# Kernel optimization log

Hardware: AMD Instinct MI355X
Metric: run time of the kernel (lower is better)

## Reference

```python
import jax, jax.numpy as jnp
import numpy as np

N_NODES = 100000
N_EDGES = 1600000
IN_C, HID_C, OUT_C = 32, 64, 32


def setup_inputs() -> dict:
    key = jax.random.key(0)
    ks = jax.random.split(key, 8)
    x = jax.random.normal(ks[0], (N_NODES, IN_C), dtype=jnp.float32)
    edge_index = jax.random.randint(ks[1], (2, N_EDGES), 0, N_NODES, dtype=jnp.int64)
    s = 1.0 / np.sqrt(IN_C)
    W1_l = jax.random.uniform(ks[2], (IN_C, HID_C), jnp.float32, -s, s)
    W1_r = jax.random.uniform(ks[3], (IN_C, HID_C), jnp.float32, -s, s)
    b1 = jnp.zeros((HID_C,), jnp.float32)
    s2 = 1.0 / np.sqrt(HID_C)
    W2_l = jax.random.uniform(ks[4], (HID_C, OUT_C), jnp.float32, -s2, s2)
    W2_r = jax.random.uniform(ks[5], (HID_C, OUT_C), jnp.float32, -s2, s2)
    b2 = jnp.zeros((OUT_C,), jnp.float32)
    return {"x": x, "edge_index": edge_index, "W1_l": W1_l, "b1": b1,
            "W1_r": W1_r, "W2_l": W2_l, "b2": b2, "W2_r": W2_r}


def _sage_conv(x, src, dst, W_l, b_l, W_r):
    # mean-aggregate source features onto destination nodes (PyG SAGEConv)
    n = x.shape[0]
    agg = jax.ops.segment_sum(x[src], dst, num_segments=n)  # [N, C]
    cnt = jax.ops.segment_sum(jnp.ones_like(dst, dtype=x.dtype), dst, num_segments=n)
    agg = agg / jnp.maximum(cnt, 1.0)[:, None]
    return agg @ W_l + b_l + x @ W_r


def reference(x, edge_index, W1_l, b1, W1_r, W2_l, b2, W2_r):
    src, dst = edge_index[0], edge_index[1]
    h = jax.nn.relu(_sage_conv(x, src, dst, W1_l, b1, W1_r))
    # dropout omitted (eval mode, deterministic baseline)
    out = _sage_conv(h, src, dst, W2_l, b2, W2_r)
    return out
```

## Files before the change

kernel.cpp:

```cpp
#include <hip/hip_runtime.h>
#include <hip/hip_bf16.h>


#define BUCKET_SHIFT 8
#define BUCKET_SPAN  256
#define BUCKET_CAP   8192
#define PART_ITEMS   32
#define PART_TILE    (256 * PART_ITEMS)

__global__ __launch_bounds__(256) void partition_kernel(
        const int* __restrict__ src, const int* __restrict__ dst,
        int* __restrict__ cursorB, int* __restrict__ edgesB, int E, int nbuck) {
    __shared__ int hist[512];
    __shared__ int rank_[512];
    __shared__ int base[512];
    const int tid = threadIdx.x;
    const int tbase = blockIdx.x * PART_TILE;

    for (int i = tid; i < 512; i += 256) { hist[i] = 0; rank_[i] = 0; }
    __syncthreads();

#pragma unroll
    for (int it = 0; it < PART_ITEMS; ++it) {
        int idx = tbase + it * 256 + tid;
        if (idx < E) atomicAdd(&hist[dst[idx] >> BUCKET_SHIFT], 1);
    }
    __syncthreads();

    for (int i = tid; i < nbuck; i += 256) {
        int h = hist[i];
        base[i] = h ? atomicAdd(&cursorB[i], h) : 0;
    }
    __syncthreads();

#pragma unroll
    for (int it = 0; it < PART_ITEMS; ++it) {
        int idx = tbase + it * 256 + tid;
        if (idx < E) {
            int d = dst[idx];
            int b = d >> BUCKET_SHIFT;
            int ld = d & (BUCKET_SPAN - 1);
            int r = atomicAdd(&rank_[b], 1);
            edgesB[(size_t)b * BUCKET_CAP + base[b] + r] = (ld << 24) | src[idx];
        }
    }
}

__global__ __launch_bounds__(512) void bucket_scan_kernel(
        const int* __restrict__ cursorB, int* __restrict__ bucketStart, int nbuck) {
    __shared__ int s[512];
    int t = threadIdx.x;
    int v = (t < nbuck) ? cursorB[t] : 0;
    s[t] = v;
    __syncthreads();
    for (int off = 1; off < 512; off <<= 1) {
        int a = (t >= off) ? s[t - off] : 0;
        __syncthreads();
        s[t] += a;
        __syncthreads();
    }
    if (t < nbuck) bucketStart[t] = s[t] - v;
}

__global__ __launch_bounds__(256) void bucket_csr_kernel(
        const int* __restrict__ cursorB, const int* __restrict__ bucketStart,
        const int* __restrict__ edgesB, int* __restrict__ row_start,
        int* __restrict__ sorted_src, int N, int nbuck) {
    __shared__ int cnt[BUCKET_SPAN];
    __shared__ int cur[BUCKET_SPAN];
    __shared__ int sc[BUCKET_SPAN];
    __shared__ int sorted[BUCKET_CAP];

    const int b = blockIdx.x;
    const int t = threadIdx.x;
    const int nodeBase = b << BUCKET_SHIFT;
    const int span = min(BUCKET_SPAN, N - nodeBase);
    const int size = cursorB[b];
    const int gstart = bucketStart[b];
    const int* eb = edgesB + (size_t)b * BUCKET_CAP;

    cnt[t] = 0;
    __syncthreads();
    for (int i = t; i < size; i += 256) atomicAdd(&cnt[((unsigned)eb[i]) >> 24], 1);
    __syncthreads();

    sc[t] = cnt[t];
    __syncthreads();
    for (int off = 1; off < BUCKET_SPAN; off <<= 1) {
        int a = (t >= off) ? sc[t - off] : 0;
        __syncthreads();
        sc[t] += a;
        __syncthreads();
    }
    int excl = sc[t] - cnt[t];
    if (t < span) row_start[nodeBase + t] = gstart + excl;
    if (b == nbuck - 1 && t == 0) row_start[N] = gstart + size;
    cur[t] = excl;
    __syncthreads();

    for (int i = t; i < size; i += 256) {
        int p = eb[i];
        int r = atomicAdd(&cur[((unsigned)p) >> 24], 1);
        sorted[r] = p & 0xFFFFFF;
    }
    __syncthreads();
    for (int i = t; i < size; i += 256) sorted_src[gstart + i] = sorted[i];
}

__global__ __launch_bounds__(512) void layer1_kernel(
        const float* __restrict__ x, const int* __restrict__ row_start,
        const int* __restrict__ sorted_src,
        const float* __restrict__ W1l, const float* __restrict__ b1,
        const float* __restrict__ W1r, const float* __restrict__ W2l,
        const float* __restrict__ W2r, const float* __restrict__ b2,
        float* __restrict__ hW, float* __restrict__ d2, int N) {
    __shared__ float sW1l[32 * 64];
    __shared__ float sW1r[32 * 64];
    __shared__ float sW2l[64 * 32];
    __shared__ float sW2r[64 * 32];
    __shared__ float sb1[64], sb2[32];
    __shared__ float sAgg[8][32], sX[8][32], sH[8][64];

    {
        int t = threadIdx.x;
        ((float4*)sW1l)[t] = ((const float4*)W1l)[t];
        ((float4*)sW1r)[t] = ((const float4*)W1r)[t];
        ((float4*)sW2l)[t] = ((const float4*)W2l)[t];
        ((float4*)sW2r)[t] = ((const float4*)W2r)[t];
        if (t < 64) sb1[t] = b1[t];
        if (t < 32) sb2[t] = b2[t];
    }
    __syncthreads();

    const int w = threadIdx.x >> 6;
    const int lane = threadIdx.x & 63;
    const int n = blockIdx.x * 8 + w;
    if (n >= N) return;

    const int sub = lane & 7;
    const int rowi = lane >> 3;

    int rs = row_start[n];
    int re = row_start[n + 1];
    int deg = re - rs;
    float inv = 1.0f / fmaxf((float)deg, 1.0f);
    const int* sp = sorted_src + rs;
    const float4* x4 = (const float4*)x;

    float4 acc = make_float4(0.f, 0.f, 0.f, 0.f);
    int j = 0;
    for (; j + 8 <= deg; j += 8) {
        int e = sp[j + rowi];
        float4 v = x4[(size_t)e * 8 + sub];
        acc.x += v.x; acc.y += v.y; acc.z += v.z; acc.w += v.w;
    }
    int rem = deg - j;
    if (rowi < rem) {
        int e = sp[j + rowi];
        float4 v = x4[(size_t)e * 8 + sub];
        acc.x += v.x; acc.y += v.y; acc.z += v.z; acc.w += v.w;
    }
#pragma unroll
    for (int off = 8; off < 64; off <<= 1) {
        acc.x += __shfl_xor(acc.x, off);
        acc.y += __shfl_xor(acc.y, off);
        acc.z += __shfl_xor(acc.z, off);
        acc.w += __shfl_xor(acc.w, off);
    }
    if (lane < 8) {
        float4 m;
        m.x = acc.x * inv; m.y = acc.y * inv; m.z = acc.z * inv; m.w = acc.w * inv;
        ((float4*)sAgg[w])[lane] = m;
        ((float4*)sX[w])[lane] = x4[(size_t)n * 8 + lane];
    }

    float accd = sb1[lane];
#pragma unroll
    for (int k = 0; k < 32; ++k)
        accd += sAgg[w][k] * sW1l[k * 64 + lane] + sX[w][k] * sW1r[k * 64 + lane];
    float hv = fmaxf(accd, 0.0f);
    sH[w][lane] = hv;

    const int c2 = lane & 31;
    const int half = lane >> 5;
    float p1 = 0.f, p2 = 0.f;
#pragma unroll
    for (int kk = 0; kk < 32; ++kk) {
        int k = half * 32 + kk;
        float hk = sH[w][k];
        p1 += hk * sW2l[k * 32 + c2];
        p2 += hk * sW2r[k * 32 + c2];
    }
    p1 += __shfl_xor(p1, 32);
    p2 += __shfl_xor(p2, 32);
    if (lane < 32) {
        hW[(size_t)n * 32 + c2] = p1;
        d2[(size_t)n * 32 + c2] = p2 + sb2[c2];
    }
}

__global__ __launch_bounds__(256) void layer2_kernel(
        const float* __restrict__ hW, const float* __restrict__ d2,
        const int* __restrict__ row_start, const int* __restrict__ sorted_src,
        float* __restrict__ out, int N) {
    const int w = threadIdx.x >> 6;
    const int lane = threadIdx.x & 63;
    const int n = blockIdx.x * 4 + w;
    if (n >= N) return;

    const int sub = lane & 7;
    const int rowi = lane >> 3;
    int rs = row_start[n];
    int re = row_start[n + 1];
    int deg = re - rs;
    float inv = 1.0f / fmaxf((float)deg, 1.0f);
    const int* sp = sorted_src + rs;
    const float4* t4 = (const float4*)hW;

    float4 acc = make_float4(0.f, 0.f, 0.f, 0.f);
    int j = 0;
    for (; j + 8 <= deg; j += 8) {
        int e = sp[j + rowi];
        float4 v = t4[(size_t)e * 8 + sub];
        acc.x += v.x; acc.y += v.y; acc.z += v.z; acc.w += v.w;
    }
    int rem = deg - j;
    if (rowi < rem) {
        int e = sp[j + rowi];
        float4 v = t4[(size_t)e * 8 + sub];
        acc.x += v.x; acc.y += v.y; acc.z += v.z; acc.w += v.w;
    }
#pragma unroll
    for (int off = 8; off < 64; off <<= 1) {
        acc.x += __shfl_xor(acc.x, off);
        acc.y += __shfl_xor(acc.y, off);
        acc.z += __shfl_xor(acc.z, off);
        acc.w += __shfl_xor(acc.w, off);
    }
    if (lane < 8) {
        float4 dd = ((const float4*)d2)[(size_t)n * 8 + lane];
        float4 o;
        o.x = acc.x * inv + dd.x;
        o.y = acc.y * inv + dd.y;
        o.z = acc.z * inv + dd.z;
        o.w = acc.w * inv + dd.w;
        ((float4*)out)[(size_t)n * 8 + lane] = o;
    }
}

extern "C" void kernel_launch(void* const* d_in, const int* in_sizes, int n_in,
                              void* d_out, int out_size, void* d_ws, size_t ws_size,
                              hipStream_t stream) {
    const float* x   = (const float*)d_in[0];
    const int*   ei  = (const int*)d_in[1];
    const float* W1l = (const float*)d_in[2];
    const float* b1  = (const float*)d_in[3];
    const float* W1r = (const float*)d_in[4];
    const float* W2l = (const float*)d_in[5];
    const float* b2  = (const float*)d_in[6];
    const float* W2r = (const float*)d_in[7];
    float* out = (float*)d_out;

    const int N = in_sizes[0] / 32;
    const int E = in_sizes[1] / 2;
    const int* src = ei;
    const int* dst = ei + E;
    const int NBUCK = (N + BUCKET_SPAN - 1) >> BUCKET_SHIFT;

    char* p = (char*)d_ws;
    auto align64 = [](size_t v) { return (v + 63) & ~(size_t)63; };
    int* cursorB     = (int*)p;   p += align64((size_t)NBUCK * 4);
    int* bucketStart = (int*)p;   p += align64((size_t)(NBUCK + 1) * 4);
    int* row_start   = (int*)p;   p += align64((size_t)(N + 1) * 4);
    int* sorted_src  = (int*)p;   p += align64((size_t)E * 4);
    int* edgesB      = (int*)p;   p += align64((size_t)NBUCK * BUCKET_CAP * 4);
    float* hW        = (float*)p; p += align64((size_t)N * 32 * 4);
    float* d2        = (float*)p; p += align64((size_t)N * 32 * 4);

    hipMemsetAsync(cursorB, 0, (size_t)NBUCK * 4, stream);

    int ntiles = (E + PART_TILE - 1) / PART_TILE;
    partition_kernel<<<ntiles, 256, 0, stream>>>(src, dst, cursorB, edgesB, E, NBUCK);
    bucket_scan_kernel<<<1, 512, 0, stream>>>(cursorB, bucketStart, NBUCK);
    bucket_csr_kernel<<<NBUCK, 256, 0, stream>>>(cursorB, bucketStart, edgesB,
                                                 row_start, sorted_src, N, NBUCK);

    layer1_kernel<<<(N + 7) / 8, 512, 0, stream>>>(x, row_start, sorted_src,
                                                   W1l, b1, W1r, W2l, W2r, b2,
                                                   hW, d2, N);
    layer2_kernel<<<(N + 3) / 4, 256, 0, stream>>>(hW, d2, row_start, sorted_src,
                                                   out, N);
}
```

Measured before the change: 278.2 us.

## Store layer-2 gather table in fp16 and batch neighbor index loads per wave

The intermediate hW table read by the layer-2 neighbor gather is now stored in half precision, which halves the bytes moved by that random-access gather. Both gathers now load up to 64 neighbor indices with one coalesced read, hand them out by wave shuffle, and issue eight independent row loads before accumulating, so more memory requests are in flight at once. The cost is fp16 rounding of hW before aggregation, which adds numerical error, plus extra registers per thread.

```diff
diff --git a/kernel.cpp b/kernel.cpp
--- a/kernel.cpp
+++ b/kernel.cpp
@@ -1,5 +1,6 @@
 #include <hip/hip_runtime.h>
 #include <hip/hip_bf16.h>
+#include <hip/hip_fp16.h>
 
 
 #define BUCKET_SHIFT 8
@@ -107,13 +108,85 @@
     for (int i = t; i < size; i += 256) sorted_src[gstart + i] = sorted[i];
 }
 
+__device__ __forceinline__ float4 gather_sum_f32(const float4* __restrict__ t4,
+                                                 const int* __restrict__ sp,
+                                                 int deg, int lane) {
+    const int sub = lane & 7;
+    const int rowi = lane >> 3;
+    float4 acc = make_float4(0.f, 0.f, 0.f, 0.f);
+    for (int base = 0; base < deg; base += 64) {
+        int chunk = min(deg - base, 64);
+        int myidx = (lane < chunk) ? sp[base + lane] : -1;
+        int nit = (chunk + 7) >> 3;
+        int e[8];
+        float4 v[8];
+#pragma unroll
+        for (int it = 0; it < 8; ++it)
+            e[it] = (it < nit) ? __shfl(myidx, it * 8 + rowi) : -1;
+#pragma unroll
+        for (int it = 0; it < 8; ++it)
+            v[it] = (e[it] >= 0) ? t4[(size_t)e[it] * 8 + sub]
+                                 : make_float4(0.f, 0.f, 0.f, 0.f);
+#pragma unroll
+        for (int it = 0; it < 8; ++it) {
+            acc.x += v[it].x; acc.y += v[it].y;
+            acc.z += v[it].z; acc.w += v[it].w;
+        }
+    }
+#pragma unroll
+    for (int off = 8; off < 64; off <<= 1) {
+        acc.x += __shfl_xor(acc.x, off);
+        acc.y += __shfl_xor(acc.y, off);
+        acc.z += __shfl_xor(acc.z, off);
+        acc.w += __shfl_xor(acc.w, off);
+    }
+    return acc;
+}
+
+__device__ __forceinline__ float4 gather_sum_f16(const float2* __restrict__ t2,
+                                                 const int* __restrict__ sp,
+                                                 int deg, int lane) {
+    const int sub = lane & 7;
+    const int rowi = lane >> 3;
+    float4 acc = make_float4(0.f, 0.f, 0.f, 0.f);
+    for (int base = 0; base < deg; base += 64) {
+        int chunk = min(deg - base, 64);
+        int myidx = (lane < chunk) ? sp[base + lane] : -1;
+        int nit = (chunk + 7) >> 3;
+        int e[8];
+        float2 v[8];
+#pragma unroll
+        for (int it = 0; it < 8; ++it)
+            e[it] = (it < nit) ? __shfl(myidx, it * 8 + rowi) : -1;
+#pragma unroll
+        for (int it = 0; it < 8; ++it)
+            v[it] = (e[it] >= 0) ? t2[(size_t)e[it] * 8 + sub]
+                                 : make_float2(0.f, 0.f);
+#pragma unroll
+        for (int it = 0; it < 8; ++it) {
+            const __half2* hp = (const __half2*)&v[it];
+            float2 lo = __half22float2(hp[0]);
+            float2 hi = __half22float2(hp[1]);
+            acc.x += lo.x; acc.y += lo.y; acc.z += hi.x; acc.w += hi.y;
+        }
+    }
+#pragma unroll
+    for (int off = 8; off < 64; off <<= 1) {
+        acc.x += __shfl_xor(acc.x, off);
+        acc.y += __shfl_xor(acc.y, off);
+        acc.z += __shfl_xor(acc.z, off);
+        acc.w += __shfl_xor(acc.w, off);
+    }
+    return acc;
+}
+
 __global__ __launch_bounds__(512) void layer1_kernel(
         const float* __restrict__ x, const int* __restrict__ row_start,
         const int* __restrict__ sorted_src,
         const float* __restrict__ W1l, const float* __restrict__ b1,
         const float* __restrict__ W1r, const float* __restrict__ W2l,
         const float* __restrict__ W2r, const float* __restrict__ b2,
-        float* __restrict__ hW, float* __restrict__ d2, int N) {
+        __half* __restrict__ hWh, float* __restrict__ d2, int N) {
     __shared__ float sW1l[32 * 64];
     __shared__ float sW1r[32 * 64];
     __shared__ float sW2l[64 * 32];
@@ -137,36 +210,14 @@
     const int n = blockIdx.x * 8 + w;
     if (n >= N) return;
 
-    const int sub = lane & 7;
-    const int rowi = lane >> 3;
-
     int rs = row_start[n];
     int re = row_start[n + 1];
     int deg = re - rs;
     float inv = 1.0f / fmaxf((float)deg, 1.0f);
-    const int* sp = sorted_src + rs;
     const float4* x4 = (const float4*)x;
 
-    float4 acc = make_float4(0.f, 0.f, 0.f, 0.f);
-    int j = 0;
-    for (; j + 8 <= deg; j += 8) {
-        int e = sp[j + rowi];
-        float4 v = x4[(size_t)e * 8 + sub];
-        acc.x += v.x; acc.y += v.y; acc.z += v.z; acc.w += v.w;
-    }
-    int rem = deg - j;
-    if (rowi < rem) {
-        int e = sp[j + rowi];
-        float4 v = x4[(size_t)e * 8 + sub];
-        acc.x += v.x; acc.y += v.y; acc.z += v.z; acc.w += v.w;
-    }
-#pragma unroll
-    for (int off = 8; off < 64; off <<= 1) {
-        acc.x += __shfl_xor(acc.x, off);
-        acc.y += __shfl_xor(acc.y, off);
-        acc.z += __shfl_xor(acc.z, off);
-        acc.w += __shfl_xor(acc.w, off);
-    }
+    float4 acc = gather_sum_f32(x4, sorted_src + rs, deg, lane);
+
     if (lane < 8) {
         float4 m;
         m.x = acc.x * inv; m.y = acc.y * inv; m.z = acc.z * inv; m.w = acc.w * inv;
@@ -194,13 +245,13 @@
     p1 += __shfl_xor(p1, 32);
     p2 += __shfl_xor(p2, 32);
     if (lane < 32) {
-        hW[(size_t)n * 32 + c2] = p1;
+        hWh[(size_t)n * 32 + c2] = __float2half_rn(p1);
         d2[(size_t)n * 32 + c2] = p2 + sb2[c2];
     }
 }
 
 __global__ __launch_bounds__(256) void layer2_kernel(
-        const float* __restrict__ hW, const float* __restrict__ d2,
+        const __half* __restrict__ hWh, const float* __restrict__ d2,
         const int* __restrict__ row_start, const int* __restrict__ sorted_src,
         float* __restrict__ out, int N) {
     const int w = threadIdx.x >> 6;
@@ -208,35 +259,13 @@
     const int n = blockIdx.x * 4 + w;
     if (n >= N) return;
 
-    const int sub = lane & 7;
-    const int rowi = lane >> 3;
     int rs = row_start[n];
     int re = row_start[n + 1];
     int deg = re - rs;
     float inv = 1.0f / fmaxf((float)deg, 1.0f);
-    const int* sp = sorted_src + rs;
-    const float4* t4 = (const float4*)hW;
-
-    float4 acc = make_float4(0.f, 0.f, 0.f, 0.f);
-    int j = 0;
-    for (; j + 8 <= deg; j += 8) {
-        int e = sp[j + rowi];
-        float4 v = t4[(size_t)e * 8 + sub];
-        acc.x += v.x; acc.y += v.y; acc.z += v.z; acc.w += v.w;
-    }
-    int rem = deg - j;
-    if (rowi < rem) {
-        int e = sp[j + rowi];
-        float4 v = t4[(size_t)e * 8 + sub];
-        acc.x += v.x; acc.y += v.y; acc.z += v.z; acc.w += v.w;
-    }
-#pragma unroll
-    for (int off = 8; off < 64; off <<= 1) {
-        acc.x += __shfl_xor(acc.x, off);
-        acc.y += __shfl_xor(acc.y, off);
-        acc.z += __shfl_xor(acc.z, off);
-        acc.w += __shfl_xor(acc.w, off);
-    }
+
+    float4 acc = gather_sum_f16((const float2*)hWh, sorted_src + rs, deg, lane);
+
     if (lane < 8) {
         float4 dd = ((const float4*)d2)[(size_t)n * 8 + lane];
         float4 o;
@@ -269,13 +298,13 @@
 
     char* p = (char*)d_ws;
     auto align64 = [](size_t v) { return (v + 63) & ~(size_t)63; };
-    int* cursorB     = (int*)p;   p += align64((size_t)NBUCK * 4);
-    int* bucketStart = (int*)p;   p += align64((size_t)(NBUCK + 1) * 4);
-    int* row_start   = (int*)p;   p += align64((size_t)(N + 1) * 4);
-    int* sorted_src  = (int*)p;   p += align64((size_t)E * 4);
-    int* edgesB      = (int*)p;   p += align64((size_t)NBUCK * BUCKET_CAP * 4);
-    float* hW        = (float*)p; p += align64((size_t)N * 32 * 4);
-    float* d2        = (float*)p; p += align64((size_t)N * 32 * 4);
+    int* cursorB     = (int*)p;    p += align64((size_t)NBUCK * 4);
+    int* bucketStart = (int*)p;    p += align64((size_t)(NBUCK + 1) * 4);
+    int* row_start   = (int*)p;    p += align64((size_t)(N + 1) * 4);
+    int* sorted_src  = (int*)p;    p += align64((size_t)E * 4);
+    int* edgesB      = (int*)p;    p += align64((size_t)NBUCK * BUCKET_CAP * 4);
+    __half* hWh      = (__half*)p; p += align64((size_t)N * 32 * 2);
+    float* d2        = (float*)p;  p += align64((size_t)N * 32 * 4);
 
     hipMemsetAsync(cursorB, 0, (size_t)NBUCK * 4, stream);
 
@@ -287,7 +316,7 @@
 
     layer1_kernel<<<(N + 7) / 8, 512, 0, stream>>>(x, row_start, sorted_src,
                                                    W1l, b1, W1r, W2l, W2r, b2,
-                                                   hW, d2, N);
-    layer2_kernel<<<(N + 3) / 4, 256, 0, stream>>>(hW, d2, row_start, sorted_src,
+                                                   hWh, d2, N);
+    layer2_kernel<<<(N + 3) / 4, 256, 0, stream>>>(hWh, d2, row_start, sorted_src,
                                                    out, N);
 }
```

Result: faster. 263.3 us (-5.3%).

## Aggregate directly from dst buckets with LDS atomics, drop CSR build, fp16 hW

Applied to the files above, without the earlier changes.

Removes the bucket scan and CSR construction kernels. Aggregation now runs per 256-node bucket, accumulating gathered features into shared memory with atomics. Layer 1 aggregation is split into its own kernel that writes mean features and inverse degrees, followed by a dense kernel that applies the MLP. The layer-2 intermediate is stored as fp16 to halve gather bandwidth, at some precision cost. The trade-off is heavy LDS float atomics and extra global round trips for aggM, in exchange for skipping the sort passes.

```diff
diff --git a/kernel.cpp b/kernel.cpp
--- a/kernel.cpp
+++ b/kernel.cpp
@@ -1,5 +1,6 @@
 #include <hip/hip_runtime.h>
 #include <hip/hip_bf16.h>
+#include <hip/hip_fp16.h>
 
 
 #define BUCKET_SHIFT 8
@@ -10,7 +11,7 @@
 
 __global__ __launch_bounds__(256) void partition_kernel(
         const int* __restrict__ src, const int* __restrict__ dst,
-        int* __restrict__ cursorB, int* __restrict__ edgesB, int E, int nbuck) {
+        int* __restrict__ cursorB, unsigned* __restrict__ edgesB, int E, int nbuck) {
     __shared__ int hist[512];
     __shared__ int rank_[512];
     __shared__ int base[512];
@@ -39,81 +40,80 @@
         if (idx < E) {
             int d = dst[idx];
             int b = d >> BUCKET_SHIFT;
-            int ld = d & (BUCKET_SPAN - 1);
+            unsigned ld = (unsigned)(d & (BUCKET_SPAN - 1));
             int r = atomicAdd(&rank_[b], 1);
-            edgesB[(size_t)b * BUCKET_CAP + base[b] + r] = (ld << 24) | src[idx];
-        }
-    }
-}
-
-__global__ __launch_bounds__(512) void bucket_scan_kernel(
-        const int* __restrict__ cursorB, int* __restrict__ bucketStart, int nbuck) {
-    __shared__ int s[512];
-    int t = threadIdx.x;
-    int v = (t < nbuck) ? cursorB[t] : 0;
-    s[t] = v;
-    __syncthreads();
-    for (int off = 1; off < 512; off <<= 1) {
-        int a = (t >= off) ? s[t - off] : 0;
-        __syncthreads();
-        s[t] += a;
-        __syncthreads();
-    }
-    if (t < nbuck) bucketStart[t] = s[t] - v;
-}
-
-__global__ __launch_bounds__(256) void bucket_csr_kernel(
-        const int* __restrict__ cursorB, const int* __restrict__ bucketStart,
-        const int* __restrict__ edgesB, int* __restrict__ row_start,
-        int* __restrict__ sorted_src, int N, int nbuck) {
-    __shared__ int cnt[BUCKET_SPAN];
-    __shared__ int cur[BUCKET_SPAN];
-    __shared__ int sc[BUCKET_SPAN];
-    __shared__ int sorted[BUCKET_CAP];
+            edgesB[(size_t)b * BUCKET_CAP + base[b] + r] =
+                (ld << 24) | (unsigned)src[idx];
+        }
+    }
+}
+
+__global__ __launch_bounds__(512) void agg1_kernel(
+        const float* __restrict__ x, const unsigned* __restrict__ edgesB,
+        const int* __restrict__ cursorB,
+        float* __restrict__ aggM, float* __restrict__ invG, int N) {
+    __shared__ float sAgg[BUCKET_SPAN * 32];
+    __shared__ int sCnt[BUCKET_SPAN];
 
     const int b = blockIdx.x;
-    const int t = threadIdx.x;
+    const int tid = threadIdx.x;
+    const int size = cursorB[b];
+    const unsigned* eb = edgesB + (size_t)b * BUCKET_CAP;
+
+    for (int i = tid; i < BUCKET_SPAN * 8; i += 512)
+        ((float4*)sAgg)[i] = make_float4(0.f, 0.f, 0.f, 0.f);
+    if (tid < BUCKET_SPAN) sCnt[tid] = 0;
+    __syncthreads();
+
+    const int sub = tid & 7;
+    const int slot = tid >> 3;
+    const float4* x4 = (const float4*)x;
+
+    for (int base2 = 0; base2 < size; base2 += 256) {
+        unsigned p[4]; bool k[4]; float4 v[4];
+#pragma unroll
+        for (int u = 0; u < 4; ++u) {
+            int i = base2 + u * 64 + slot;
+            k[u] = i < size;
+            p[u] = k[u] ? eb[i] : 0u;
+        }
+#pragma unroll
+        for (int u = 0; u < 4; ++u)
+            v[u] = k[u] ? x4[(size_t)(p[u] & 0xFFFFFFu) * 8 + sub]
+                        : make_float4(0.f, 0.f, 0.f, 0.f);
+#pragma unroll
+        for (int u = 0; u < 4; ++u) {
+            if (k[u]) {
+                float* ap = sAgg + (p[u] >> 24) * 32 + sub * 4;
+                atomicAdd(ap + 0, v[u].x);
+                atomicAdd(ap + 1, v[u].y);
+                atomicAdd(ap + 2, v[u].z);
+                atomicAdd(ap + 3, v[u].w);
+                if (sub == 0) atomicAdd(&sCnt[p[u] >> 24], 1);
+            }
+        }
+    }
+    __syncthreads();
+
     const int nodeBase = b << BUCKET_SHIFT;
     const int span = min(BUCKET_SPAN, N - nodeBase);
-    const int size = cursorB[b];
-    const int gstart = bucketStart[b];
-    const int* eb = edgesB + (size_t)b * BUCKET_CAP;
-
-    cnt[t] = 0;
-    __syncthreads();
-    for (int i = t; i < size; i += 256) atomicAdd(&cnt[((unsigned)eb[i]) >> 24], 1);
-    __syncthreads();
-
-    sc[t] = cnt[t];
-    __syncthreads();
-    for (int off = 1; off < BUCKET_SPAN; off <<= 1) {
-        int a = (t >= off) ? sc[t - off] : 0;
-        __syncthreads();
-        sc[t] += a;
-        __syncthreads();
-    }
-    int excl = sc[t] - cnt[t];
-    if (t < span) row_start[nodeBase + t] = gstart + excl;
-    if (b == nbuck - 1 && t == 0) row_start[N] = gstart + size;
-    cur[t] = excl;
-    __syncthreads();
-
-    for (int i = t; i < size; i += 256) {
-        int p = eb[i];
-        int r = atomicAdd(&cur[((unsigned)p) >> 24], 1);
-        sorted[r] = p & 0xFFFFFF;
-    }
-    __syncthreads();
-    for (int i = t; i < size; i += 256) sorted_src[gstart + i] = sorted[i];
-}
-
-__global__ __launch_bounds__(512) void layer1_kernel(
-        const float* __restrict__ x, const int* __restrict__ row_start,
-        const int* __restrict__ sorted_src,
+    for (int u = tid; u < span * 8; u += 512) {
+        int node = u >> 3;
+        float inv = 1.0f / fmaxf((float)sCnt[node], 1.0f);
+        float4 a = ((float4*)sAgg)[u];
+        a.x *= inv; a.y *= inv; a.z *= inv; a.w *= inv;
+        ((float4*)aggM)[(size_t)nodeBase * 8 + u] = a;
+    }
+    for (int t = tid; t < span; t += 512)
+        invG[nodeBase + t] = 1.0f / fmaxf((float)sCnt[t], 1.0f);
+}
+
+__global__ __launch_bounds__(512) void dense_kernel(
+        const float* __restrict__ x, const float* __restrict__ aggM,
         const float* __restrict__ W1l, const float* __restrict__ b1,
         const float* __restrict__ W1r, const float* __restrict__ W2l,
         const float* __restrict__ W2r, const float* __restrict__ b2,
-        float* __restrict__ hW, float* __restrict__ d2, int N) {
+        __half* __restrict__ hWh, float* __restrict__ d2, int N) {
     __shared__ float sW1l[32 * 64];
     __shared__ float sW1r[32 * 64];
     __shared__ float sW2l[64 * 32];
@@ -137,41 +137,9 @@
     const int n = blockIdx.x * 8 + w;
     if (n >= N) return;
 
-    const int sub = lane & 7;
-    const int rowi = lane >> 3;
-
-    int rs = row_start[n];
-    int re = row_start[n + 1];
-    int deg = re - rs;
-    float inv = 1.0f / fmaxf((float)deg, 1.0f);
-    const int* sp = sorted_src + rs;
-    const float4* x4 = (const float4*)x;
-
-    float4 acc = make_float4(0.f, 0.f, 0.f, 0.f);
-    int j = 0;
-    for (; j + 8 <= deg; j += 8) {
-        int e = sp[j + rowi];
-        float4 v = x4[(size_t)e * 8 + sub];
-        acc.x += v.x; acc.y += v.y; acc.z += v.z; acc.w += v.w;
-    }
-    int rem = deg - j;
-    if (rowi < rem) {
-        int e = sp[j + rowi];
-        float4 v = x4[(size_t)e * 8 + sub];
-        acc.x += v.x; acc.y += v.y; acc.z += v.z; acc.w += v.w;
-    }
-#pragma unroll
-    for (int off = 8; off < 64; off <<= 1) {
-        acc.x += __shfl_xor(acc.x, off);
-        acc.y += __shfl_xor(acc.y, off);
-        acc.z += __shfl_xor(acc.z, off);
-        acc.w += __shfl_xor(acc.w, off);
-    }
     if (lane < 8) {
-        float4 m;
-        m.x = acc.x * inv; m.y = acc.y * inv; m.z = acc.z * inv; m.w = acc.w * inv;
-        ((float4*)sAgg[w])[lane] = m;
-        ((float4*)sX[w])[lane] = x4[(size_t)n * 8 + lane];
+        ((float4*)sAgg[w])[lane] = ((const float4*)aggM)[(size_t)n * 8 + lane];
+        ((float4*)sX[w])[lane] = ((const float4*)x)[(size_t)n * 8 + lane];
     }
 
     float accd = sb1[lane];
@@ -194,57 +162,70 @@
     p1 += __shfl_xor(p1, 32);
     p2 += __shfl_xor(p2, 32);
     if (lane < 32) {
-        hW[(size_t)n * 32 + c2] = p1;
+        hWh[(size_t)n * 32 + c2] = __float2half_rn(p1);
         d2[(size_t)n * 32 + c2] = p2 + sb2[c2];
     }
 }
 
-__global__ __launch_bounds__(256) void layer2_kernel(
-        const float* __restrict__ hW, const float* __restrict__ d2,
-        const int* __restrict__ row_start, const int* __restrict__ sorted_src,
-        float* __restrict__ out, int N) {
-    const int w = threadIdx.x >> 6;
-    const int lane = threadIdx.x & 63;
-    const int n = blockIdx.x * 4 + w;
-    if (n >= N) return;
-
-    const int sub = lane & 7;
-    const int rowi = lane >> 3;
-    int rs = row_start[n];
-    int re = row_start[n + 1];
-    int deg = re - rs;
-    float inv = 1.0f / fmaxf((float)deg, 1.0f);
-    const int* sp = sorted_src + rs;
-    const float4* t4 = (const float4*)hW;
-
-    float4 acc = make_float4(0.f, 0.f, 0.f, 0.f);
-    int j = 0;
-    for (; j + 8 <= deg; j += 8) {
-        int e = sp[j + rowi];
-        float4 v = t4[(size_t)e * 8 + sub];
-        acc.x += v.x; acc.y += v.y; acc.z += v.z; acc.w += v.w;
-    }
-    int rem = deg - j;
-    if (rowi < rem) {
-        int e = sp[j + rowi];
-        float4 v = t4[(size_t)e * 8 + sub];
-        acc.x += v.x; acc.y += v.y; acc.z += v.z; acc.w += v.w;
-    }
-#pragma unroll
-    for (int off = 8; off < 64; off <<= 1) {
-        acc.x += __shfl_xor(acc.x, off);
-        acc.y += __shfl_xor(acc.y, off);
-        acc.z += __shfl_xor(acc.z, off);
-        acc.w += __shfl_xor(acc.w, off);
-    }
-    if (lane < 8) {
-        float4 dd = ((const float4*)d2)[(size_t)n * 8 + lane];
-        float4 o;
-        o.x = acc.x * inv + dd.x;
-        o.y = acc.y * inv + dd.y;
-        o.z = acc.z * inv + dd.z;
-        o.w = acc.w * inv + dd.w;
-        ((float4*)out)[(size_t)n * 8 + lane] = o;
+__global__ __launch_bounds__(512) void agg2_kernel(
+        const __half* __restrict__ hWh, const unsigned* __restrict__ edgesB,
+        const int* __restrict__ cursorB, const float* __restrict__ invG,
+        const float* __restrict__ d2, float* __restrict__ out, int N) {
+    __shared__ float sAgg[BUCKET_SPAN * 32];
+
+    const int b = blockIdx.x;
+    const int tid = threadIdx.x;
+    const int size = cursorB[b];
+    const unsigned* eb = edgesB + (size_t)b * BUCKET_CAP;
+
+    for (int i = tid; i < BUCKET_SPAN * 8; i += 512)
+        ((float4*)sAgg)[i] = make_float4(0.f, 0.f, 0.f, 0.f);
+    __syncthreads();
+
+    const int sub = tid & 7;
+    const int slot = tid >> 3;
+    const float2* h2 = (const float2*)hWh;
+
+    for (int base2 = 0; base2 < size; base2 += 256) {
+        unsigned p[4]; bool k[4]; float2 r[4];
+#pragma unroll
+        for (int u = 0; u < 4; ++u) {
+            int i = base2 + u * 64 + slot;
+            k[u] = i < size;
+            p[u] = k[u] ? eb[i] : 0u;
+        }
+#pragma unroll
+        for (int u = 0; u < 4; ++u)
+            r[u] = k[u] ? h2[(size_t)(p[u] & 0xFFFFFFu) * 8 + sub]
+                        : make_float2(0.f, 0.f);
+#pragma unroll
+        for (int u = 0; u < 4; ++u) {
+            if (k[u]) {
+                const __half2* hp = (const __half2*)&r[u];
+                float2 lo = __half22float2(hp[0]);
+                float2 hi = __half22float2(hp[1]);
+                float* ap = sAgg + (p[u] >> 24) * 32 + sub * 4;
+                atomicAdd(ap + 0, lo.x);
+                atomicAdd(ap + 1, lo.y);
+                atomicAdd(ap + 2, hi.x);
+                atomicAdd(ap + 3, hi.y);
+            }
+        }
+    }
+    __syncthreads();
+
+    const int nodeBase = b << BUCKET_SHIFT;
+    const int span = min(BUCKET_SPAN, N - nodeBase);
+    for (int u = tid; u < span * 8; u += 512) {
+        int node = u >> 3;
+        float inv = invG[nodeBase + node];
+        float4 a = ((float4*)sAgg)[u];
+        float4 dd = ((const float4*)d2)[(size_t)nodeBase * 8 + u];
+        a.x = a.x * inv + dd.x;
+        a.y = a.y * inv + dd.y;
+        a.z = a.z * inv + dd.z;
+        a.w = a.w * inv + dd.w;
+        ((float4*)out)[(size_t)nodeBase * 8 + u] = a;
     }
 }
 
@@ -269,25 +250,19 @@
 
     char* p = (char*)d_ws;
     auto align64 = [](size_t v) { return (v + 63) & ~(size_t)63; };
-    int* cursorB     = (int*)p;   p += align64((size_t)NBUCK * 4);
-    int* bucketStart = (int*)p;   p += align64((size_t)(NBUCK + 1) * 4);
-    int* row_start   = (int*)p;   p += align64((size_t)(N + 1) * 4);
-    int* sorted_src  = (int*)p;   p += align64((size_t)E * 4);
-    int* edgesB      = (int*)p;   p += align64((size_t)NBUCK * BUCKET_CAP * 4);
-    float* hW        = (float*)p; p += align64((size_t)N * 32 * 4);
-    float* d2        = (float*)p; p += align64((size_t)N * 32 * 4);
+    int* cursorB      = (int*)p;      p += align64((size_t)NBUCK * 4);
+    unsigned* edgesB  = (unsigned*)p; p += align64((size_t)NBUCK * BUCKET_CAP * 4);
+    float* aggM       = (float*)p;    p += align64((size_t)N * 32 * 4);
+    float* invG       = (float*)p;    p += align64((size_t)N * 4);
+    __half* hWh       = (__half*)p;   p += align64((size_t)N * 32 * 2);
+    float* d2         = (float*)p;    p += align64((size_t)N * 32 * 4);
 
     hipMemsetAsync(cursorB, 0, (size_t)NBUCK * 4, stream);
 
     int ntiles = (E + PART_TILE - 1) / PART_TILE;
     partition_kernel<<<ntiles, 256, 0, stream>>>(src, dst, cursorB, edgesB, E, NBUCK);
-    bucket_scan_kernel<<<1, 512, 0, stream>>>(cursorB, bucketStart, NBUCK);
-    bucket_csr_kernel<<<NBUCK, 256, 0, stream>>>(cursorB, bucketStart, edgesB,
-                                                 row_start, sorted_src, N, NBUCK);
-
-    layer1_kernel<<<(N + 7) / 8, 512, 0, stream>>>(x, row_start, sorted_src,
-                                                   W1l, b1, W1r, W2l, W2r, b2,
-                                                   hW, d2, N);
-    layer2_kernel<<<(N + 3) / 4, 256, 0, stream>>>(hW, d2, row_start, sorted_src,
-                                                   out, N);
-}
+    agg1_kernel<<<NBUCK, 512, 0, stream>>>(x, edgesB, cursorB, aggM, invG, N);
+    dense_kernel<<<(N + 7) / 8, 512, 0, stream>>>(x, aggM, W1l, b1, W1r,
+                                                  W2l, W2r, b2, hWh, d2, N);
+    agg2_kernel<<<NBUCK, 512, 0, stream>>>(hWh, edgesB, cursorB, invG, d2, out, N);
+}
```

After: 886.4 us. +218.7%, slower.
